# Performance work log

Hardware: AMD Instinct MI355X
Metric: run time of the kernel (lower is better)

## Reference

```python
import jax, jax.numpy as jnp
import numpy as np

D_MODEL = 1024
NUM_HEADS = 16
HEAD_DIM = D_MODEL // NUM_HEADS


def setup_inputs() -> dict:
    key = jax.random.key(0)
    k1, k2, k3 = jax.random.split(key, 3)
    x = jax.random.normal(k1, (2, 2048, D_MODEL), dtype=jnp.float32)
    a_qkv = (6.0 / (D_MODEL + 3 * D_MODEL)) ** 0.5
    w_qkv = jax.random.uniform(k2, (3 * D_MODEL, D_MODEL), jnp.float32, -a_qkv, a_qkv)
    a_p = (6.0 / (D_MODEL + D_MODEL)) ** 0.5
    w_proj = jax.random.uniform(k3, (D_MODEL, D_MODEL), jnp.float32, -a_p, a_p)
    return {"in_features": x, "w_qkv": w_qkv, "w_proj": w_proj}


def reference(in_features, w_qkv, w_proj):
    B, S, _ = in_features.shape
    qkv = jnp.einsum('bsi,ji->bsj', in_features, w_qkv)  # [B,S,3*D]
    # split (3, head, d_k) from last dim, -> [3, B, H, S, d_k]
    qkv = qkv.reshape(B, S, 3, NUM_HEADS, HEAD_DIM)
    qkv = jnp.transpose(qkv, (2, 0, 3, 1, 4))
    q, k, v = qkv[0], qkv[1], qkv[2]
    q = q * (HEAD_DIM ** -0.5)
    weight = jnp.einsum('bhqd,bhkd->bhqk', q, k)  # [B,H,S,S]
    causal = jnp.tril(jnp.ones((S, S), dtype=bool))
    weight = jnp.where(causal, weight, -jnp.inf)
    score = jax.nn.softmax(weight, axis=-1)
    attn = jnp.einsum('bhqk,bhkd->bhqd', score, v)
    attn = jnp.transpose(attn, (0, 2, 1, 3)).reshape(B, S, D_MODEL)
    return jnp.einsum('bsi,ji->bsj', attn, w_proj)
```

## Files before the change

kernel.cpp:

```cpp
#include <hip/hip_runtime.h>

#define S_LEN 2048
#define DM 1024
#define NH 16
#define HD 64
#define QKV_LD 3072

using f32x4 = __attribute__((ext_vector_type(4))) float;
using s16x8 = __attribute__((ext_vector_type(8))) short;

__device__ __forceinline__ unsigned short f2bf(float f) {
  union { float f; unsigned u; } v; v.f = f;
  unsigned r = v.u + 0x7fffu + ((v.u >> 16) & 1u);
  return (unsigned short)(r >> 16);
}

__device__ __forceinline__ float bf2f(unsigned short u) {
  union { unsigned u; float f; } v; v.u = ((unsigned)u) << 16;
  return v.f;
}

__device__ __forceinline__ void gload_lds16(const void* g, void* l) {
  __builtin_amdgcn_global_load_lds(
      (const __attribute__((address_space(1))) void*)g,
      (__attribute__((address_space(3))) void*)l, 16, 0, 0);
}

__global__ __launch_bounds__(256) void cvt_f32_bf16(const float* __restrict__ in,
                                                    unsigned short* __restrict__ out,
                                                    int n) {
  int i = (blockIdx.x * 256 + threadIdx.x) * 8;
  if (i >= n) return;
  float4 a = *(const float4*)(in + i);
  float4 b = *(const float4*)(in + i + 4);
  s16x8 o;
  o[0] = f2bf(a.x); o[1] = f2bf(a.y); o[2] = f2bf(a.z); o[3] = f2bf(a.w);
  o[4] = f2bf(b.x); o[5] = f2bf(b.y); o[6] = f2bf(b.z); o[7] = f2bf(b.w);
  *(s16x8*)(out + i) = o;
}

template <bool OUT_F32>
__global__ __launch_bounds__(256, 2) void gemm_bt(const unsigned short* __restrict__ A,
                                                  const unsigned short* __restrict__ W,
                                                  void* __restrict__ Cout,
                                                  int M, int N, int K, int nbn) {
  __shared__ unsigned short As[128 * 64];
  __shared__ unsigned short Bs[128 * 64];
  const int bm = blockIdx.x / nbn, bn = blockIdx.x % nbn;
  const int tid = threadIdx.x;
  const int w = tid >> 6, lane = tid & 63;
  const int wr = w >> 1, wc = w & 1;
  const int lr = lane & 15, lk = lane >> 4;
  const int m0 = bm * 128, n0 = bn * 128;
  f32x4 acc[4][4] = {};

  for (int k0 = 0; k0 < K; k0 += 64) {
#pragma unroll
    for (int i = 0; i < 4; ++i) {
      const int base = i * 4096 + w * 1024;
      const int boff = base + lane * 16;
      const int row = boff >> 7;
      const int col = (boff >> 1) & 63;
      gload_lds16(A + (size_t)(m0 + row) * K + k0 + col, (char*)As + base);
      gload_lds16(W + (size_t)(n0 + row) * K + k0 + col, (char*)Bs + base);
    }
    __syncthreads();
#pragma unroll
    for (int kk = 0; kk < 2; ++kk) {
      s16x8 af[4], bfr[4];
#pragma unroll
      for (int m = 0; m < 4; ++m)
        af[m] = *(const s16x8*)((const char*)As + (wr * 64 + m * 16 + lr) * 128 + kk * 64 + lk * 16);
#pragma unroll
      for (int n = 0; n < 4; ++n)
        bfr[n] = *(const s16x8*)((const char*)Bs + (wc * 64 + n * 16 + lr) * 128 + kk * 64 + lk * 16);
#pragma unroll
      for (int m = 0; m < 4; ++m)
#pragma unroll
        for (int n = 0; n < 4; ++n)
          acc[m][n] = __builtin_amdgcn_mfma_f32_16x16x32_bf16(af[m], bfr[n], acc[m][n], 0, 0, 0);
    }
    __syncthreads();
  }
#pragma unroll
  for (int m = 0; m < 4; ++m)
#pragma unroll
    for (int n = 0; n < 4; ++n)
#pragma unroll
      for (int r = 0; r < 4; ++r) {
        const int row = m0 + wr * 64 + m * 16 + lk * 4 + r;
        const int col = n0 + wc * 64 + n * 16 + lr;
        if (OUT_F32)
          ((float*)Cout)[(size_t)row * N + col] = acc[m][n][r];
        else
          ((unsigned short*)Cout)[(size_t)row * N + col] = f2bf(acc[m][n][r]);
      }
}

__global__ __launch_bounds__(256) void vtrans(const unsigned short* __restrict__ qkv,
                                              unsigned short* __restrict__ vt) {
  __shared__ unsigned short T[64][65];
  const int blk = blockIdx.x;
  const int st = blk & 31, bh = blk >> 5;
  const int h = bh & 15, b = bh >> 4;
  const int s0 = st * 64;
  const int tid = threadIdx.x;
#pragma unroll
  for (int i = 0; i < 2; ++i) {
    const int idx = tid + i * 256;
    const int sy = idx >> 3, tx = idx & 7;
    s16x8 v = *(const s16x8*)(qkv + (size_t)(b * S_LEN + s0 + sy) * QKV_LD + 2 * DM + h * HD + tx * 8);
#pragma unroll
    for (int j = 0; j < 8; ++j) T[tx * 8 + j][sy] = v[j];
  }
  __syncthreads();
#pragma unroll
  for (int i = 0; i < 2; ++i) {
    const int idx = tid + i * 256;
    const int d = idx >> 3, tx = idx & 7;
    s16x8 v;
#pragma unroll
    for (int j = 0; j < 8; ++j) v[j] = T[d][tx * 8 + j];
    *(s16x8*)(vt + (size_t)bh * (HD * S_LEN) + (size_t)d * S_LEN + s0 + tx * 8) = v;
  }
}

__global__ __launch_bounds__(256, 4) void attn_fwd(const unsigned short* __restrict__ qkv,
                                                   const unsigned short* __restrict__ vt,
                                                   unsigned short* __restrict__ aout) {
  __shared__ unsigned short Ks[64 * 64];
  __shared__ unsigned short Vs[64 * 64];
  __shared__ unsigned short Pbuf[4][16][72];
  const int bid = blockIdx.x;
  const int qt = 31 - (bid >> 5);
  const int bh = bid & 31;
  const int h = bh & 15, b = bh >> 4;
  const int tid = threadIdx.x, w = tid >> 6, lane = tid & 63;
  const int lr = lane & 15, lk = lane >> 4;
  const int qb = qt * 64 + w * 16;
  const size_t rowbase = (size_t)b * S_LEN;
  const unsigned short* kbase = qkv + rowbase * QKV_LD + DM + h * HD;
  const unsigned short* vbase = vt + (size_t)bh * (HD * S_LEN);

  const int r8 = lane >> 3, c8 = lane & 7;
  const int celem = ((c8 ^ r8) << 3);

  const int swz = (lr & 7) << 3;

  s16x8 qf[2];
#pragma unroll
  for (int dk = 0; dk < 2; ++dk) {
    s16x8 q = *(const s16x8*)(qkv + (rowbase + qb + lr) * QKV_LD + h * HD + dk * 32 + lk * 8);
#pragma unroll
    for (int j = 0; j < 8; ++j)
      q[j] = (short)f2bf(bf2f((unsigned short)q[j]) * 0.18033688011112042f);
    qf[dk] = q;
  }

  f32x4 oacc[4] = {};
  float mr = -1e30f, ls = 0.f;

  for (int t = 0; t <= qt; ++t) {
    const int k0 = t * 64;
#pragma unroll
    for (int jj = 0; jj < 4; ++jj) {
      const int j = w * 4 + jj;
      if (j < 8) {
        gload_lds16(kbase + (size_t)(k0 + j * 8 + r8) * QKV_LD + celem,
                    (char*)Ks + j * 1024);
      } else {
        gload_lds16(vbase + (size_t)((j - 8) * 8 + r8) * S_LEN + k0 + celem,
                    (char*)Vs + (j - 8) * 1024);
      }
    }
    __syncthreads();

    const bool dtile = (t == qt);
    f32x4 sf[4];
#pragma unroll
    for (int n = 0; n < 4; ++n) {
      if (!dtile || n <= w) {
        s16x8 kf0 = *(const s16x8*)(Ks + (n * 16 + lr) * 64 + ((lk * 8) ^ swz));
        s16x8 kf1 = *(const s16x8*)(Ks + (n * 16 + lr) * 64 + ((32 + lk * 8) ^ swz));
        f32x4 s = {};
        s = __builtin_amdgcn_mfma_f32_16x16x32_bf16(kf0, qf[0], s, 0, 0, 0);
        s = __builtin_amdgcn_mfma_f32_16x16x32_bf16(kf1, qf[1], s, 0, 0, 0);
        sf[n] = s;
      } else {
#pragma unroll
        for (int r = 0; r < 4; ++r) sf[n][r] = -1e30f;
      }
    }
    if (dtile) {
#pragma unroll
      for (int r = 0; r < 4; ++r)
        if (lk * 4 + r > lr) sf[w][r] = -1e30f;
    }
    float pm = sf[0][0];
#pragma unroll
    for (int n = 0; n < 4; ++n)
#pragma unroll
      for (int r = 0; r < 4; ++r) pm = fmaxf(pm, sf[n][r]);
    pm = fmaxf(pm, __shfl_xor(pm, 16));
    pm = fmaxf(pm, __shfl_xor(pm, 32));
    if (__any(pm > mr + 8.f)) {
      const float mn = fmaxf(mr, pm);
      const float al = __builtin_amdgcn_exp2f(mr - mn);
      mr = mn;
      ls *= al;
#pragma unroll
      for (int r = 0; r < 4; ++r) {
        const float alq = __shfl(al, lk * 4 + r);
#pragma unroll
        for (int n = 0; n < 4; ++n) oacc[n][r] *= alq;
      }
    }
    float rs = 0.f;
#pragma unroll
    for (int n = 0; n < 4; ++n)
#pragma unroll
      for (int r = 0; r < 4; ++r) {
        const float p = __builtin_amdgcn_exp2f(sf[n][r] - mr);
        sf[n][r] = p;
        rs += p;
      }
    rs += __shfl_xor(rs, 16);
    rs += __shfl_xor(rs, 32);
    ls += rs;
#pragma unroll
    for (int n = 0; n < 4; ++n) {
      union { float f; unsigned u; } c0, c1, c2, c3;
      c0.f = sf[n][0]; c1.f = sf[n][1]; c2.f = sf[n][2]; c3.f = sf[n][3];
      uint2 pk;
      pk.x = ((c0.u + 0x8000u) >> 16) | (((c1.u + 0x8000u) >> 16) << 16);
      pk.y = ((c2.u + 0x8000u) >> 16) | (((c3.u + 0x8000u) >> 16) << 16);
      *(uint2*)&Pbuf[w][lr][n * 16 + lk * 4] = pk;
    }
#pragma unroll
    for (int kk = 0; kk < 2; ++kk) {
      s16x8 pf = *(const s16x8*)&Pbuf[w][lr][kk * 32 + lk * 8];
#pragma unroll
      for (int n = 0; n < 4; ++n) {
        s16x8 vf = *(const s16x8*)(Vs + (n * 16 + lr) * 64 + ((kk * 32 + lk * 8) ^ swz));
        oacc[n] = __builtin_amdgcn_mfma_f32_16x16x32_bf16(pf, vf, oacc[n], 0, 0, 0);
      }
    }
    __syncthreads();
  }

  const float rl = __builtin_amdgcn_rcpf(ls);
#pragma unroll
  for (int r = 0; r < 4; ++r) {
    const float rlq = __shfl(rl, lk * 4 + r);
#pragma unroll
    for (int n = 0; n < 4; ++n)
      aout[(rowbase + qb + lk * 4 + r) * DM + h * HD + n * 16 + lr] = f2bf(oacc[n][r] * rlq);
  }
}

extern "C" void kernel_launch(void* const* d_in, const int* in_sizes, int n_in,
                              void* d_out, int out_size, void* d_ws, size_t ws_size,
                              hipStream_t stream) {
  const float* x = (const float*)d_in[0];
  const float* wqkv = (const float*)d_in[1];
  const float* wproj = (const float*)d_in[2];
  float* out = (float*)d_out;

  char* ws = (char*)d_ws;
  unsigned short* xb = (unsigned short*)ws;
  unsigned short* wqkvb = (unsigned short*)(ws + (8u << 20));
  unsigned short* wprojb = (unsigned short*)(ws + (14u << 20));
  unsigned short* vtb = (unsigned short*)ws;
  unsigned short* qkvb = (unsigned short*)(ws + (16u << 20));
  unsigned short* attnb = (unsigned short*)(ws + (40u << 20));

  cvt_f32_bf16<<<2048, 256, 0, stream>>>(x, xb, 4096 * 1024);
  cvt_f32_bf16<<<1536, 256, 0, stream>>>(wqkv, wqkvb, 3072 * 1024);

  gemm_bt<false><<<32 * 24, 256, 0, stream>>>(xb, wqkvb, qkvb, 4096, 3072, 1024, 24);
  vtrans<<<1024, 256, 0, stream>>>(qkvb, vtb);
  attn_fwd<<<1024, 256, 0, stream>>>(qkvb, vtb, attnb);
  cvt_f32_bf16<<<512, 256, 0, stream>>>(wproj, wprojb, 1024 * 1024);
  gemm_bt<true><<<32 * 8, 256, 0, stream>>>(attnb, wprojb, out, 4096, 1024, 1024, 8);
}
```

Before: 188.5 us.

## Double-buffer K/V tiles in LDS and raise MFMA wave priority

Doubles the K and V shared-memory tiles so the asynchronous global-to-LDS load of the next key tile is issued before computing on the current one. This overlaps load latency with the QK^T and PV matrix work. It also wraps the MFMA sections in s_setprio to favour waves doing matrix work. The extra LDS lowers the launch-bounds occupancy hint from 4 to 3 blocks per CU.

```diff
diff --git a/kernel.cpp b/kernel.cpp
--- a/kernel.cpp
+++ b/kernel.cpp
@@ -125,11 +125,11 @@
   }
 }
 
-__global__ __launch_bounds__(256, 4) void attn_fwd(const unsigned short* __restrict__ qkv,
+__global__ __launch_bounds__(256, 3) void attn_fwd(const unsigned short* __restrict__ qkv,
                                                    const unsigned short* __restrict__ vt,
                                                    unsigned short* __restrict__ aout) {
-  __shared__ unsigned short Ks[64 * 64];
-  __shared__ unsigned short Vs[64 * 64];
+  __shared__ unsigned short Ks[2][64 * 64];
+  __shared__ unsigned short Vs[2][64 * 64];
   __shared__ unsigned short Pbuf[4][16][72];
   const int bid = blockIdx.x;
   const int qt = 31 - (bid >> 5);
@@ -144,7 +144,6 @@
 
   const int r8 = lane >> 3, c8 = lane & 7;
   const int celem = ((c8 ^ r8) << 3);
-
   const int swz = (lr & 7) << 3;
 
   s16x8 qf[2];
@@ -160,28 +159,36 @@
   f32x4 oacc[4] = {};
   float mr = -1e30f, ls = 0.f;
 
+  auto stage = [&](int t, int c) {
+    const int k0 = t * 64;
+#pragma unroll
+    for (int jj = 0; jj < 4; ++jj) {
+      const int j = w * 4 + jj;
+      if (j < 8)
+        gload_lds16(kbase + (size_t)(k0 + j * 8 + r8) * QKV_LD + celem,
+                    (char*)Ks[c] + j * 1024);
+      else
+        gload_lds16(vbase + (size_t)((j - 8) * 8 + r8) * S_LEN + k0 + celem,
+                    (char*)Vs[c] + (j - 8) * 1024);
+    }
+  };
+
+  stage(0, 0);
+  __syncthreads();
+  int c = 0;
+
   for (int t = 0; t <= qt; ++t) {
     const int k0 = t * 64;
-#pragma unroll
-    for (int jj = 0; jj < 4; ++jj) {
-      const int j = w * 4 + jj;
-      if (j < 8) {
-        gload_lds16(kbase + (size_t)(k0 + j * 8 + r8) * QKV_LD + celem,
-                    (char*)Ks + j * 1024);
-      } else {
-        gload_lds16(vbase + (size_t)((j - 8) * 8 + r8) * S_LEN + k0 + celem,
-                    (char*)Vs + (j - 8) * 1024);
-      }
-    }
-    __syncthreads();
+    if (t < qt) stage(t + 1, c ^ 1);
 
     const bool dtile = (t == qt);
     f32x4 sf[4];
+    __builtin_amdgcn_s_setprio(1);
 #pragma unroll
     for (int n = 0; n < 4; ++n) {
       if (!dtile || n <= w) {
-        s16x8 kf0 = *(const s16x8*)(Ks + (n * 16 + lr) * 64 + ((lk * 8) ^ swz));
-        s16x8 kf1 = *(const s16x8*)(Ks + (n * 16 + lr) * 64 + ((32 + lk * 8) ^ swz));
+        s16x8 kf0 = *(const s16x8*)(Ks[c] + (n * 16 + lr) * 64 + ((lk * 8) ^ swz));
+        s16x8 kf1 = *(const s16x8*)(Ks[c] + (n * 16 + lr) * 64 + ((32 + lk * 8) ^ swz));
         f32x4 s = {};
         s = __builtin_amdgcn_mfma_f32_16x16x32_bf16(kf0, qf[0], s, 0, 0, 0);
         s = __builtin_amdgcn_mfma_f32_16x16x32_bf16(kf1, qf[1], s, 0, 0, 0);
@@ -191,6 +198,7 @@
         for (int r = 0; r < 4; ++r) sf[n][r] = -1e30f;
       }
     }
+    __builtin_amdgcn_s_setprio(0);
     if (dtile) {
 #pragma unroll
       for (int r = 0; r < 4; ++r)
@@ -236,16 +244,19 @@
       pk.y = ((c2.u + 0x8000u) >> 16) | (((c3.u + 0x8000u) >> 16) << 16);
       *(uint2*)&Pbuf[w][lr][n * 16 + lk * 4] = pk;
     }
+    __builtin_amdgcn_s_setprio(1);
 #pragma unroll
     for (int kk = 0; kk < 2; ++kk) {
       s16x8 pf = *(const s16x8*)&Pbuf[w][lr][kk * 32 + lk * 8];
 #pragma unroll
       for (int n = 0; n < 4; ++n) {
-        s16x8 vf = *(const s16x8*)(Vs + (n * 16 + lr) * 64 + ((kk * 32 + lk * 8) ^ swz));
+        s16x8 vf = *(const s16x8*)(Vs[c] + (n * 16 + lr) * 64 + ((kk * 32 + lk * 8) ^ swz));
         oacc[n] = __builtin_amdgcn_mfma_f32_16x16x32_bf16(pf, vf, oacc[n], 0, 0, 0);
       }
     }
+    __builtin_amdgcn_s_setprio(0);
     __syncthreads();
+    c ^= 1;
   }
 
   const float rl = __builtin_amdgcn_rcpf(ls);
```

After: 188.9 us. About the same (+0.2%).
